# Performance work log

Measured on AMD Instinct MI355X. Metric: run time of the kernel, lower is better.

## Reference

```python
import jax, jax.numpy as jnp
import numpy as np


def setup_inputs() -> dict:
    key = jax.random.key(0)
    k1, k2 = jax.random.split(key)
    B, N, M = 2, 8192, 8192
    source_point_cloud = jax.random.normal(k1, (B, N, 3), dtype=jnp.float32)
    target_point_cloud = jax.random.normal(k2, (B, M, 3), dtype=jnp.float32)
    return {"source_point_cloud": source_point_cloud,
            "target_point_cloud": target_point_cloud}


def reference(source_point_cloud, target_point_cloud):
    # source: [B, N, 3], target: [B, M, 3]
    s, t = source_point_cloud, target_point_cloud
    # Brute-force exact 1-NN (replaces per-batch CPU cKDTree query).
    # ||s - t||^2 = ||s||^2 + ||t||^2 - 2 s.t ; argmin unaffected by const terms per row,
    # but keep ||t||^2 since it varies over the argmin axis.
    s2 = jnp.sum(s * s, axis=-1)                       # [B, N]
    t2 = jnp.sum(t * t, axis=-1)                       # [B, M]
    dots = jnp.einsum('bnd,bmd->bnm', s, t)            # [B, N, M]
    d2 = t2[:, None, :] - 2.0 * dots                   # [B, N, M] (drop s2: row-constant)
    idx = jnp.argmin(d2, axis=-1)                      # [B, N] nearest target index
    target_points = jnp.take_along_axis(t, idx[..., None], axis=1)  # [B, N, 3]
    # MSELoss (mean over all elements) per batch, then mean over batch.
    per_batch = jnp.mean((s - target_points) ** 2, axis=(1, 2))     # [B]
    return jnp.mean(per_batch)
```

## Files before the change

kernel.cpp:

```cpp
#include <hip/hip_runtime.h>

#define BLOCK  256
#define SPT    16
#define NSLICE 256
#define UN     8

typedef float vfloat2 __attribute__((ext_vector_type(2)));

__global__ __launch_bounds__(256) void prep_kernel(
    const float* __restrict__ tgt, float4* __restrict__ tpre,
    float* __restrict__ out, int M, int Mp, int total)
{
    int i = blockIdx.x * 256 + threadIdx.x;
    if (i == 0) out[0] = 0.f;
    if (i >= total) return;
    int b = i / Mp, m = i - b * Mp;
    float x = 0.f, y = 0.f, z = 0.f, t2 = 1e30f;
    if (m < M) {
        const float* p = tgt + ((size_t)b * M + m) * 3;
        x = p[0]; y = p[1]; z = p[2];
        t2 = fmaf(x, x, fmaf(y, y, z * z));
    }
    tpre[i] = make_float4(x, y, z, t2);
}

__global__ __launch_bounds__(BLOCK) void chamfer_min_kernel(
    const float* __restrict__ src, const float4* __restrict__ tpre,
    float* __restrict__ out, int N, int Mp, int total_src, float scale)
{
    const int tid = threadIdx.x;
    const int sbase = blockIdx.x * SPT;
    const int b = (sbase < total_src) ? (sbase / N) : 0;
    const float* sb = src + (size_t)b * N * 3;
    const float4* tb = tpre + (size_t)b * Mp;

    vfloat2 nsx2[SPT], nsy2[SPT], nsz2[SPT];
    float s2[SPT], mind[SPT];
    unsigned vmask = 0;
#pragma unroll
    for (int u = 0; u < SPT; ++u) {
        int gsi = sbase + u;
        int si  = gsi - b * N;
        bool ok = (gsi < total_src) && (si >= 0) && (si < N);
        if (ok) vmask |= (1u << u);
        float x = 0.f, y = 0.f, z = 0.f;
        if (ok) {
            x = sb[(size_t)si * 3 + 0];
            y = sb[(size_t)si * 3 + 1];
            z = sb[(size_t)si * 3 + 2];
        }
        nsx2[u] = (vfloat2){-2.f * x, -2.f * x};
        nsy2[u] = (vfloat2){-2.f * y, -2.f * y};
        nsz2[u] = (vfloat2){-2.f * z, -2.f * z};
        s2[u]   = fmaf(x, x, fmaf(y, y, z * z));
        mind[u] = 1e30f;
    }

    const int TPT = Mp / NSLICE;
    for (int k0 = 0; k0 < TPT; k0 += UN) {
        float4 t[UN];
#pragma unroll
        for (int j = 0; j < UN; ++j) {
            t[j] = tb[(size_t)(k0 + j) * NSLICE + tid];
        }
#pragma unroll
        for (int j = 0; j < UN; j += 2) {
            vfloat2 cx = {t[j].x, t[j + 1].x};
            vfloat2 cy = {t[j].y, t[j + 1].y};
            vfloat2 cz = {t[j].z, t[j + 1].z};
            vfloat2 cw = {t[j].w, t[j + 1].w};
#pragma unroll
            for (int u = 0; u < SPT; ++u) {
                vfloat2 d = __builtin_elementwise_fma(nsx2[u], cx,
                            __builtin_elementwise_fma(nsy2[u], cy,
                            __builtin_elementwise_fma(nsz2[u], cz, cw)));
                mind[u] = fminf(mind[u], fminf(d.x, d.y));
            }
        }
    }

#pragma unroll
    for (int u = 0; u < SPT; ++u) {
#pragma unroll
        for (int off = 1; off < 64; off <<= 1) {
            mind[u] = fminf(mind[u], __shfl_xor(mind[u], off, 64));
        }
    }

    __shared__ float red[BLOCK / 64][SPT];
    const int lane = tid & 63;
    const int w    = tid >> 6;
    if (lane == 0) {
#pragma unroll
        for (int u = 0; u < SPT; ++u) red[w][u] = mind[u];
    }
    __syncthreads();

    if (tid == 0) {
        float ssum = 0.f;
#pragma unroll
        for (int u = 0; u < SPT; ++u) {
            float mv = red[0][u];
#pragma unroll
            for (int ww = 1; ww < BLOCK / 64; ++ww) mv = fminf(mv, red[ww][u]);
            if (vmask & (1u << u)) ssum += s2[u] + mv;
        }
        atomicAdd(out, ssum * scale);
    }
}

extern "C" void kernel_launch(void* const* d_in, const int* in_sizes, int n_in,
                              void* d_out, int out_size, void* d_ws, size_t ws_size,
                              hipStream_t stream) {
    const float* src = (const float*)d_in[0];
    const float* tgt = (const float*)d_in[1];
    float* out = (float*)d_out;

    const int B = 2;
    const int N = in_sizes[0] / (B * 3);
    const int M = in_sizes[1] / (B * 3);
    const int total_src = B * N;

    const int step = NSLICE * UN;
    const int Mp = ((M + step - 1) / step) * step;
    float4* tpre = (float4*)d_ws;

    const int prep_total = B * Mp;
    prep_kernel<<<(prep_total + 255) / 256, 256, 0, stream>>>(
        tgt, tpre, out, M, Mp, prep_total);

    const int grid = (total_src + SPT - 1) / SPT;
    chamfer_min_kernel<<<grid, BLOCK, 0, stream>>>(
        src, tpre, out, N, Mp, total_src,
        1.0f / (3.0f * (float)N * (float)B));
}
```

Measured before the change: 77.30 us.

## Keep source coordinates in scalar registers and double-buffer target loads

Result: slower. 81.38 us (+5.3%).

```diff
diff --git a/kernel.cpp b/kernel.cpp
--- a/kernel.cpp
+++ b/kernel.cpp
@@ -6,6 +6,10 @@
 #define UN     8
 
 typedef float vfloat2 __attribute__((ext_vector_type(2)));
+
+__device__ __forceinline__ float rfl(float x) {
+    return __int_as_float(__builtin_amdgcn_readfirstlane(__float_as_int(x)));
+}
 
 __global__ __launch_bounds__(256) void prep_kernel(
     const float* __restrict__ tgt, float4* __restrict__ tpre,
@@ -34,8 +38,7 @@
     const float* sb = src + (size_t)b * N * 3;
     const float4* tb = tpre + (size_t)b * Mp;
 
-    vfloat2 nsx2[SPT], nsy2[SPT], nsz2[SPT];
-    float s2[SPT], mind[SPT];
+    float nsx[SPT], nsy[SPT], nsz[SPT], mind[SPT];
     unsigned vmask = 0;
 #pragma unroll
     for (int u = 0; u < SPT; ++u) {
@@ -49,33 +52,47 @@
             y = sb[(size_t)si * 3 + 1];
             z = sb[(size_t)si * 3 + 2];
         }
-        nsx2[u] = (vfloat2){-2.f * x, -2.f * x};
-        nsy2[u] = (vfloat2){-2.f * y, -2.f * y};
-        nsz2[u] = (vfloat2){-2.f * z, -2.f * z};
-        s2[u]   = fmaf(x, x, fmaf(y, y, z * z));
+        nsx[u] = rfl(-2.f * x);
+        nsy[u] = rfl(-2.f * y);
+        nsz[u] = rfl(-2.f * z);
         mind[u] = 1e30f;
     }
 
     const int TPT = Mp / NSLICE;
+
+    float4 tc[UN], tn[UN];
+#pragma unroll
+    for (int j = 0; j < UN; ++j) tc[j] = tb[(size_t)j * NSLICE + tid];
+
+#pragma unroll 2
     for (int k0 = 0; k0 < TPT; k0 += UN) {
-        float4 t[UN];
+        const bool more = (k0 + UN) < TPT;
+        if (more) {
 #pragma unroll
-        for (int j = 0; j < UN; ++j) {
-            t[j] = tb[(size_t)(k0 + j) * NSLICE + tid];
+            for (int j = 0; j < UN; ++j) {
+                tn[j] = tb[(size_t)(k0 + UN + j) * NSLICE + tid];
+            }
         }
 #pragma unroll
         for (int j = 0; j < UN; j += 2) {
-            vfloat2 cx = {t[j].x, t[j + 1].x};
-            vfloat2 cy = {t[j].y, t[j + 1].y};
-            vfloat2 cz = {t[j].z, t[j + 1].z};
-            vfloat2 cw = {t[j].w, t[j + 1].w};
+            vfloat2 cx = {tc[j].x, tc[j + 1].x};
+            vfloat2 cy = {tc[j].y, tc[j + 1].y};
+            vfloat2 cz = {tc[j].z, tc[j + 1].z};
+            vfloat2 cw = {tc[j].w, tc[j + 1].w};
 #pragma unroll
             for (int u = 0; u < SPT; ++u) {
-                vfloat2 d = __builtin_elementwise_fma(nsx2[u], cx,
-                            __builtin_elementwise_fma(nsy2[u], cy,
-                            __builtin_elementwise_fma(nsz2[u], cz, cw)));
+                vfloat2 sx = {nsx[u], nsx[u]};
+                vfloat2 sy = {nsy[u], nsy[u]};
+                vfloat2 sz = {nsz[u], nsz[u]};
+                vfloat2 d = __builtin_elementwise_fma(sx, cx,
+                            __builtin_elementwise_fma(sy, cy,
+                            __builtin_elementwise_fma(sz, cz, cw)));
                 mind[u] = fminf(mind[u], fminf(d.x, d.y));
             }
+        }
+        if (more) {
+#pragma unroll
+            for (int j = 0; j < UN; ++j) tc[j] = tn[j];
         }
     }
 
@@ -103,7 +120,9 @@
             float mv = red[0][u];
 #pragma unroll
             for (int ww = 1; ww < BLOCK / 64; ++ww) mv = fminf(mv, red[ww][u]);
-            if (vmask & (1u << u)) ssum += s2[u] + mv;
+            float x = -0.5f * nsx[u], y = -0.5f * nsy[u], z = -0.5f * nsz[u];
+            float s2 = fmaf(x, x, fmaf(y, y, z * z));
+            if (vmask & (1u << u)) ssum += s2 + mv;
         }
         atomicAdd(out, ssum * scale);
     }
```
